# Kernel optimization log

Measured on AMD Instinct MI355X. Metric: run time of the kernel, lower is better.

Reference implementation:

```python
import jax, jax.numpy as jnp
import numpy as np

N_NODES = 100000
N_EDGES = 1600000
N_GRAPHS = 1000
F_IN, HID = 9, 64


def _glorot(key, shape):
    fan_in, fan_out = shape[0], shape[1]
    lim = (6.0 / (fan_in + fan_out)) ** 0.5
    return jax.random.uniform(key, shape, jnp.float32, -lim, lim)


def setup_inputs() -> dict:
    key = jax.random.key(0)
    ks = jax.random.split(key, 12)
    x = jax.random.normal(ks[0], (N_NODES, F_IN), jnp.float32)
    edge_index = jax.random.randint(ks[1], (2, N_EDGES), 0, N_NODES, jnp.int64)
    edge_attr = jnp.zeros((N_EDGES, 1), jnp.float32)
    batch = jnp.sort(jax.random.randint(ks[2], (N_NODES,), 0, N_GRAPHS, jnp.int64))
    # SAGEConv layer 1: 9 -> 64 (lin_l on aggregated neighbors w/ bias, lin_r on root)
    Wl1 = _glorot(ks[3], (F_IN, HID)); Wr1 = _glorot(ks[4], (F_IN, HID)); b1 = jnp.zeros((HID,), jnp.float32)
    # SAGEConv layer 2: 64 -> 64
    Wl2 = _glorot(ks[5], (HID, HID)); Wr2 = _glorot(ks[6], (HID, HID)); b2 = jnp.zeros((HID,), jnp.float32)
    # MLP readout: 64 -> 32 -> 1
    Wm1 = _glorot(ks[7], (HID, HID // 2)); bm1 = jnp.zeros((HID // 2,), jnp.float32)
    Wm2 = _glorot(ks[8], (HID // 2, 1)); bm2 = jnp.zeros((1,), jnp.float32)
    return dict(x=x, edge_index=edge_index, edge_attr=edge_attr, batch=batch,
                Wl1=Wl1, Wr1=Wr1, b1=b1, Wl2=Wl2, Wr2=Wr2, b2=b2,
                Wm1=Wm1, bm1=bm1, Wm2=Wm2, bm2=bm2)


def _sage_conv(x, src, dst, Wl, Wr, b, n_nodes):
    # mean aggregation of source-node features onto target nodes
    msgs = x[src]                                              # [E, F] gather
    s = jax.ops.segment_sum(msgs, dst, num_segments=n_nodes)   # [N, F] scatter-add
    cnt = jax.ops.segment_sum(jnp.ones((src.shape[0],), x.dtype), dst, num_segments=n_nodes)
    agg = s / jnp.maximum(cnt, 1.0)[:, None]
    return agg @ Wl + x @ Wr + b


def reference(x, edge_index, edge_attr, batch,
              Wl1, Wr1, b1, Wl2, Wr2, b2, Wm1, bm1, Wm2, bm2):
    src, dst = edge_index[0], edge_index[1]
    n = x.shape[0]
    h = jax.nn.relu(_sage_conv(x, src, dst, Wl1, Wr1, b1, n))
    h = _sage_conv(h, src, dst, Wl2, Wr2, b2, n)               # no act after last layer
    # global mean pool over graphs
    gs = jax.ops.segment_sum(h, batch, num_segments=N_GRAPHS)
    gc = jax.ops.segment_sum(jnp.ones((n,), h.dtype), batch, num_segments=N_GRAPHS)
    xg = gs / jnp.maximum(gc, 1.0)[:, None]                    # [G, 64]
    out = jax.nn.sigmoid(jax.nn.relu(xg @ Wm1 + bm1) @ Wm2 + bm2)  # [G, 1]
    return out
```

## Files before the change

### kernel.cpp

```cpp
#include <hip/hip_runtime.h>
#include <math.h>

#define N_NODES  100000
#define N_EDGES  1600000
#define N_GRAPHS 1000
#define F_IN     9
#define HID      64
#define NBUCK    196
#define BCAP     12288
#define CHUNK    4096

typedef unsigned int uint32;
typedef float v2f __attribute__((ext_vector_type(2)));


__device__ __forceinline__ uint32 pk_lo(float a, float b, uint32 old) {
    return (uint32)__builtin_amdgcn_cvt_pk_fp8_f32(a, b, (int)old, false);
}
__device__ __forceinline__ uint32 pk_hi(float a, float b, uint32 old) {
    return (uint32)__builtin_amdgcn_cvt_pk_fp8_f32(a, b, (int)old, true);
}

__global__ __launch_bounds__(256) void pad_part_kernel(const float* __restrict__ x,
                                                       const int* __restrict__ ei,
                                                       int* __restrict__ gcur,
                                                       int2* __restrict__ ebuf,
                                                       uint32* __restrict__ x8b) {
    __shared__ int lcnt[NBUCK], lbase[NBUCK];
    int tid = threadIdx.x;

    int n = blockIdx.x * 256 + tid;
    if (n < N_NODES) {
        uint32 w[4];
        #pragma unroll
        for (int p = 0; p < 4; ++p) {
            float v0 = (4 * p + 0 < F_IN) ? x[(size_t)n * F_IN + 4 * p + 0] : 0.0f;
            float v1 = (4 * p + 1 < F_IN) ? x[(size_t)n * F_IN + 4 * p + 1] : 0.0f;
            float v2 = (4 * p + 2 < F_IN) ? x[(size_t)n * F_IN + 4 * p + 2] : 0.0f;
            float v3 = (4 * p + 3 < F_IN) ? x[(size_t)n * F_IN + 4 * p + 3] : 0.0f;
            w[p] = pk_hi(v2, v3, pk_lo(v0, v1, 0u));
        }
        *reinterpret_cast<uint4*>(&x8b[(size_t)n * 4]) =
            make_uint4(w[0], w[1], w[2], w[3]);
    }

    for (int i = tid; i < NBUCK; i += 256) lcnt[i] = 0;
    __syncthreads();
    int e0 = blockIdx.x * CHUNK;
    int e1 = e0 + CHUNK; if (e1 > N_EDGES) e1 = N_EDGES;
    for (int e = e0 + tid; e < e1; e += 256)
        atomicAdd(&lcnt[ei[N_EDGES + e] >> 9], 1);
    __syncthreads();
    for (int i = tid; i < NBUCK; i += 256)
        lbase[i] = atomicAdd(&gcur[i], lcnt[i]);
    __syncthreads();
    for (int i = tid; i < NBUCK; i += 256) lcnt[i] = 0;
    __syncthreads();
    for (int e = e0 + tid; e < e1; e += 256) {
        int src = ei[e];
        int dst = ei[N_EDGES + e];
        int b = dst >> 9;
        int pos = lbase[b] + atomicAdd(&lcnt[b], 1);
        if (pos < BCAP)
            ebuf[(size_t)b * BCAP + pos] = make_int2(src, dst);
    }
}

__global__ __launch_bounds__(512) void build_csr_kernel(const int2* __restrict__ ebuf,
                                                        const int* __restrict__ gcur,
                                                        int2* __restrict__ rowcnt,
                                                        int* __restrict__ col) {
    __shared__ int cnt[512];
    __shared__ int cur[512];
    __shared__ int wsum[8];
    int b = blockIdx.x;
    int n0 = b << 9;
    int tid = threadIdx.x;
    int ec = gcur[b]; if (ec > BCAP) ec = BCAP;
    size_t base = (size_t)b * BCAP;
    cnt[tid] = 0;
    __syncthreads();
    for (int e = tid; e < ec; e += 512)
        atomicAdd(&cnt[ebuf[base + e].y - n0], 1);
    __syncthreads();
    int v = cnt[tid];
    int lane = tid & 63, wid = tid >> 6;
    int s = v;
    #pragma unroll
    for (int off = 1; off < 64; off <<= 1) {
        int u = __shfl_up(s, off, 64);
        if (lane >= off) s += u;
    }
    if (lane == 63) wsum[wid] = s;
    __syncthreads();
    int add = 0;
    for (int w = 0; w < wid; ++w) add += wsum[w];
    int off_ex = s - v + add;
    int n = n0 + tid;
    if (n < N_NODES) rowcnt[n] = make_int2((int)base + off_ex, v);
    cur[tid] = off_ex;
    __syncthreads();
    for (int e = tid; e < ec; e += 512) {
        int2 sd = ebuf[base + e];
        int pos = atomicAdd(&cur[sd.y - n0], 1);
        col[base + pos] = sd.x;
    }
}

__global__ __launch_bounds__(256) void agg_l1_kernel(const float* __restrict__ x,
                                                     const uint32* __restrict__ x8b,
                                                     const int2* __restrict__ rowcnt,
                                                     const int* __restrict__ col,
                                                     const float* __restrict__ Wl1,
                                                     const float* __restrict__ Wr1,
                                                     const float* __restrict__ b1,
                                                     const int* __restrict__ batch,
                                                     uint32* __restrict__ h1b,
                                                     float* __restrict__ poolH) {
    __shared__ float w1s[F_IN * 128];
    __shared__ float bs[HID];
    __shared__ float ss[64 * 17];
    __shared__ float xs[64 * 10];
    __shared__ float hs[64 * 65];
    int tid = threadIdx.x;
    int n0 = blockIdx.x * 64;
    for (int i = tid; i < F_IN * HID; i += 256) {
        int f = i >> 6, j = i & 63;
        w1s[f * 128 + j]      = Wl1[i];
        w1s[f * 128 + 64 + j] = Wr1[i];
    }
    if (tid < HID) bs[tid] = b1[tid];
    for (int i = tid; i < 64 * F_IN; i += 256) {
        int r = i / F_IN, f = i - r * F_IN;
        int n = n0 + r;
        xs[r * 10 + f] = (n < N_NODES) ? x[(size_t)n * F_IN + f] : 0.0f;
    }

    {
        int r = tid >> 2, q = tid & 3;
        int n = n0 + r;
        float4 a = make_float4(0.f, 0.f, 0.f, 0.f);
        if (n < N_NODES) {
            int2 rc = rowcnt[n];
            #pragma unroll 4
            for (int i = 0; i < rc.y; ++i) {
                int c = col[rc.x + i];
                uint32 d = x8b[(size_t)c * 4 + q];
                v2f f0 = __builtin_amdgcn_cvt_pk_f32_fp8((int)d, false);
                v2f f1 = __builtin_amdgcn_cvt_pk_f32_fp8((int)d, true);
                a.x += f0[0]; a.y += f0[1];
                a.z += f1[0]; a.w += f1[1];
            }
            float inv = 1.0f / fmaxf((float)rc.y, 1.0f);
            a.x *= inv; a.y *= inv; a.z *= inv; a.w *= inv;
        }
        int q4 = q * 4;
        ss[r * 17 + q4 + 0] = a.x;
        ss[r * 17 + q4 + 1] = a.y;
        ss[r * 17 + q4 + 2] = a.z;
        ss[r * 17 + q4 + 3] = a.w;
    }
    __syncthreads();

    int r = tid >> 2, cg = tid & 3, k0 = cg * 16;
    float h[16];
    #pragma unroll
    for (int kk = 0; kk < 16; ++kk) {
        int k = k0 + kk;
        float v = bs[k];
        #pragma unroll
        for (int f = 0; f < F_IN; ++f)
            v += ss[r * 17 + f] * w1s[f * 128 + k]
               + xs[r * 10 + f] * w1s[f * 128 + 64 + k];
        v = fmaxf(v, 0.0f);
        h[kk] = v;
        hs[r * 65 + k] = v;
    }
    int n = n0 + r;
    if (n < N_NODES) {
        uint32 w[4];
        #pragma unroll
        for (int p = 0; p < 4; ++p)
            w[p] = pk_hi(h[4 * p + 2], h[4 * p + 3],
                         pk_lo(h[4 * p + 0], h[4 * p + 1], 0u));
        *reinterpret_cast<uint4*>(&h1b[(size_t)n * 16 + cg * 4]) =
            make_uint4(w[0], w[1], w[2], w[3]);
    }
    __syncthreads();
    if (tid < HID) {
        int j = tid;
        int cur = batch[(n0 < N_NODES) ? n0 : (N_NODES - 1)];
        float v = (n0 < N_NODES) ? hs[0 * 65 + j] : 0.0f;
        for (int rr = 1; rr < 64; ++rr) {
            int nn = n0 + rr;
            bool ok = (nn < N_NODES);
            int g = batch[ok ? nn : (N_NODES - 1)];
            float val = ok ? hs[rr * 65 + j] : 0.0f;
            if (g == cur) v += val;
            else { atomicAdd(&poolH[cur * HID + j], v); cur = g; v = val; }
        }
        atomicAdd(&poolH[cur * HID + j], v);
    }
}

__global__ __launch_bounds__(1024) void gather2_kernel(const uint32* __restrict__ h1b,
                                                       const int2* __restrict__ rowcnt,
                                                       const int* __restrict__ col,
                                                       const int* __restrict__ batch,
                                                       float* __restrict__ poolA) {
    __shared__ float sh[16][HID];
    int w = threadIdx.x >> 6;
    int lane = threadIdx.x & 63;
    int slot = lane >> 3;
    int grp  = lane & 7;
    int n = blockIdx.x * 16 + w;
    int2 rc = rowcnt[n];
    float a[8];
    #pragma unroll
    for (int k = 0; k < 8; ++k) a[k] = 0.0f;
    #pragma unroll 2
    for (int i = slot; i < rc.y; i += 8) {
        int c = col[rc.x + i];
        uint2 d = *reinterpret_cast<const uint2*>(&h1b[(size_t)c * 16 + grp * 2]);
        v2f f0 = __builtin_amdgcn_cvt_pk_f32_fp8((int)d.x, false);
        v2f f1 = __builtin_amdgcn_cvt_pk_f32_fp8((int)d.x, true);
        v2f f2 = __builtin_amdgcn_cvt_pk_f32_fp8((int)d.y, false);
        v2f f3 = __builtin_amdgcn_cvt_pk_f32_fp8((int)d.y, true);
        a[0] += f0[0]; a[1] += f0[1];
        a[2] += f1[0]; a[3] += f1[1];
        a[4] += f2[0]; a[5] += f2[1];
        a[6] += f3[0]; a[7] += f3[1];
    }
    #pragma unroll
    for (int k = 0; k < 8; ++k) {
        a[k] += __shfl_xor(a[k], 8, 64);
        a[k] += __shfl_xor(a[k], 16, 64);
        a[k] += __shfl_xor(a[k], 32, 64);
    }
    float inv = 1.0f / fmaxf((float)rc.y, 1.0f);
    if (slot == 0) {
        #pragma unroll
        for (int k = 0; k < 8; ++k)
            sh[w][grp * 8 + k] = a[k] * inv;
    }
    __syncthreads();
    if (threadIdx.x < HID) {
        int j = threadIdx.x;
        int base = blockIdx.x * 16;
        int cur = batch[base];
        float v = sh[0][j];
        for (int r = 1; r < 16; ++r) {
            int g = batch[base + r];
            float val = sh[r][j];
            if (g == cur) v += val;
            else { atomicAdd(&poolA[cur * HID + j], v); cur = g; v = val; }
        }
        atomicAdd(&poolA[cur * HID + j], v);
    }
}

__global__ void mlp_kernel(const float* __restrict__ poolA,
                           const float* __restrict__ poolH,
                           const int* __restrict__ batch,
                           const float* __restrict__ Wl2,
                           const float* __restrict__ Wr2,
                           const float* __restrict__ b2,
                           const float* __restrict__ Wm1,
                           const float* __restrict__ bm1,
                           const float* __restrict__ Wm2,
                           const float* __restrict__ bm2,
                           float* __restrict__ out) {
    __shared__ float spA[4][HID], spH[4][HID], sx[4][HID];
    int t = blockIdx.x * blockDim.x + threadIdx.x;
    int g = t >> 6;
    int j = t & 63;
    int w = threadIdx.x >> 6;
    if (g >= N_GRAPHS) return;
    int lo = 0, hi = N_NODES;
    while (lo < hi) { int m = (lo + hi) >> 1; if (batch[m] < g) lo = m + 1; else hi = m; }
    int start = lo;
    lo = 0; hi = N_NODES;
    while (lo < hi) { int m = (lo + hi) >> 1; if (batch[m] < g + 1) lo = m + 1; else hi = m; }
    int cntg = lo - start;
    float inv = 1.0f / fmaxf((float)cntg, 1.0f);
    spA[w][j] = poolA[g * HID + j];
    spH[w][j] = poolH[g * HID + j];
    float acc = 0.0f;
    #pragma unroll 8
    for (int k = 0; k < HID; ++k)
        acc += spA[w][k] * Wl2[k * HID + j] + spH[w][k] * Wr2[k * HID + j];
    sx[w][j] = acc * inv + b2[j];
    if (j < 32) {
        float a = bm1[j];
        #pragma unroll 8
        for (int k = 0; k < HID; ++k)
            a += sx[w][k] * Wm1[k * 32 + j];
        float r = fmaxf(a, 0.0f) * Wm2[j];
        #pragma unroll
        for (int off = 16; off > 0; off >>= 1)
            r += __shfl_down(r, off, 32);
        if (j == 0)
            out[g] = 1.0f / (1.0f + expf(-(r + bm2[0])));
    }
}

extern "C" void kernel_launch(void* const* d_in, const int* in_sizes, int n_in,
                              void* d_out, int out_size, void* d_ws, size_t ws_size,
                              hipStream_t stream) {
    const float* x    = (const float*)d_in[0];
    const int*   ei   = (const int*)d_in[1];
    const int*   batch= (const int*)d_in[3];
    const float* Wl1  = (const float*)d_in[4];
    const float* Wr1  = (const float*)d_in[5];
    const float* b1   = (const float*)d_in[6];
    const float* Wl2  = (const float*)d_in[7];
    const float* Wr2  = (const float*)d_in[8];
    const float* b2   = (const float*)d_in[9];
    const float* Wm1  = (const float*)d_in[10];
    const float* bm1  = (const float*)d_in[11];
    const float* Wm2  = (const float*)d_in[12];
    const float* bm2  = (const float*)d_in[13];
    float* out = (float*)d_out;

    int*   wsi = (int*)d_ws;
    float* wsf = (float*)d_ws;
    float*  poolA  = wsf;
    float*  poolH  = wsf + 64000;
    int*    gcur   = wsi + 128000;
    int2*   rowcnt = (int2*)(wsi + 128200);
    int*    col    = wsi + 328204;
    int2*   ebuf   = (int2*)(wsi + 2736652);
    uint32* x8b    = (uint32*)(wsi + 7553548);
    uint32* h1b    = (uint32*)(wsi + 7953548);

    hipMemsetAsync(d_ws, 0, 128200 * sizeof(int), stream);

    {   int bl = (N_EDGES + CHUNK - 1) / CHUNK;
        pad_part_kernel<<<bl, 256, 0, stream>>>(x, ei, gcur, ebuf, x8b);
    }
    build_csr_kernel<<<NBUCK, 512, 0, stream>>>(ebuf, gcur, rowcnt, col);
    {   int th = 256, bl = (N_NODES + 63) / 64;
        agg_l1_kernel<<<bl, th, 0, stream>>>(x, x8b, rowcnt, col, Wl1, Wr1, b1,
                                             batch, h1b, poolH);
    }
    {   int th = 1024, bl = N_NODES / 16;
        gather2_kernel<<<bl, th, 0, stream>>>(h1b, rowcnt, col, batch, poolA);
    }
    {   int th = 256, bl = (N_GRAPHS * 64) / th;
        mlp_kernel<<<bl, th, 0, stream>>>(poolA, poolH, batch,
                                          Wl2, Wr2, b2, Wm1, bm1, Wm2, bm2, out);
    }
}
```

Measured before the change: 154.1 us.

## Split fp8 hidden features into four column chunks to shrink the gather working set

Layer-1 outputs are now stored chunk-major: four planes of 16 fp8 features (16 bytes per node per plane) instead of 64 bytes per node row. The layer-2 gather runs four times as many blocks, each handling one feature chunk with 4-byte loads and 16 edge slots per wave. The aim is a per-pass gathered array of about 1.6 MB that stays cache-resident, which improves random-access hit rates. In exchange, col and rowcnt are re-read four times, the loads are narrower, there are four times more pooling atomics, and an extra shuffle reduction step is added.

```diff
diff --git a/kernel.cpp b/kernel.cpp
--- a/kernel.cpp
+++ b/kernel.cpp
@@ -9,6 +9,7 @@
 #define NBUCK    196
 #define BCAP     12288
 #define CHUNK    4096
+#define NGRP2    6250
 
 typedef unsigned int uint32;
 typedef float v2f __attribute__((ext_vector_type(2)));
@@ -115,7 +116,7 @@
                                                      const float* __restrict__ Wr1,
                                                      const float* __restrict__ b1,
                                                      const int* __restrict__ batch,
-                                                     uint32* __restrict__ h1b,
+                                                     uint32* __restrict__ h1c,
                                                      float* __restrict__ poolH) {
     __shared__ float w1s[F_IN * 128];
     __shared__ float bs[HID];
@@ -183,7 +184,7 @@
         for (int p = 0; p < 4; ++p)
             w[p] = pk_hi(h[4 * p + 2], h[4 * p + 3],
                          pk_lo(h[4 * p + 0], h[4 * p + 1], 0u));
-        *reinterpret_cast<uint4*>(&h1b[(size_t)n * 16 + cg * 4]) =
+        *reinterpret_cast<uint4*>(&h1c[((size_t)cg * N_NODES + n) * 4]) =
             make_uint4(w[0], w[1], w[2], w[3]);
     }
     __syncthreads();
@@ -203,36 +204,36 @@
     }
 }
 
-__global__ __launch_bounds__(1024) void gather2_kernel(const uint32* __restrict__ h1b,
+__global__ __launch_bounds__(1024) void gather2_kernel(const uint32* __restrict__ h1c,
                                                        const int2* __restrict__ rowcnt,
                                                        const int* __restrict__ col,
                                                        const int* __restrict__ batch,
                                                        float* __restrict__ poolA) {
-    __shared__ float sh[16][HID];
+    __shared__ float sh[16][16];
+    int chunk = blockIdx.x / NGRP2;
+    int ngrp  = blockIdx.x - chunk * NGRP2;
     int w = threadIdx.x >> 6;
     int lane = threadIdx.x & 63;
-    int slot = lane >> 3;
-    int grp  = lane & 7;
-    int n = blockIdx.x * 16 + w;
+    int slot = lane >> 2;
+    int dw   = lane & 3;
+    int n = ngrp * 16 + w;
     int2 rc = rowcnt[n];
-    float a[8];
+    const uint32* hbase = h1c + (size_t)chunk * N_NODES * 4 + dw;
+    float a[4];
     #pragma unroll
-    for (int k = 0; k < 8; ++k) a[k] = 0.0f;
+    for (int k = 0; k < 4; ++k) a[k] = 0.0f;
     #pragma unroll 2
-    for (int i = slot; i < rc.y; i += 8) {
+    for (int i = slot; i < rc.y; i += 16) {
         int c = col[rc.x + i];
-        uint2 d = *reinterpret_cast<const uint2*>(&h1b[(size_t)c * 16 + grp * 2]);
-        v2f f0 = __builtin_amdgcn_cvt_pk_f32_fp8((int)d.x, false);
-        v2f f1 = __builtin_amdgcn_cvt_pk_f32_fp8((int)d.x, true);
-        v2f f2 = __builtin_amdgcn_cvt_pk_f32_fp8((int)d.y, false);
-        v2f f3 = __builtin_amdgcn_cvt_pk_f32_fp8((int)d.y, true);
+        uint32 d = hbase[(size_t)c * 4];
+        v2f f0 = __builtin_amdgcn_cvt_pk_f32_fp8((int)d, false);
+        v2f f1 = __builtin_amdgcn_cvt_pk_f32_fp8((int)d, true);
         a[0] += f0[0]; a[1] += f0[1];
         a[2] += f1[0]; a[3] += f1[1];
-        a[4] += f2[0]; a[5] += f2[1];
-        a[6] += f3[0]; a[7] += f3[1];
     }
     #pragma unroll
-    for (int k = 0; k < 8; ++k) {
+    for (int k = 0; k < 4; ++k) {
+        a[k] += __shfl_xor(a[k], 4, 64);
         a[k] += __shfl_xor(a[k], 8, 64);
         a[k] += __shfl_xor(a[k], 16, 64);
         a[k] += __shfl_xor(a[k], 32, 64);
@@ -240,22 +241,23 @@
     float inv = 1.0f / fmaxf((float)rc.y, 1.0f);
     if (slot == 0) {
         #pragma unroll
-        for (int k = 0; k < 8; ++k)
-            sh[w][grp * 8 + k] = a[k] * inv;
-    }
-    __syncthreads();
-    if (threadIdx.x < HID) {
+        for (int k = 0; k < 4; ++k)
+            sh[w][dw * 4 + k] = a[k] * inv;
+    }
+    __syncthreads();
+    if (threadIdx.x < 16) {
         int j = threadIdx.x;
-        int base = blockIdx.x * 16;
+        int base = ngrp * 16;
+        int jj = chunk * 16 + j;
         int cur = batch[base];
         float v = sh[0][j];
         for (int r = 1; r < 16; ++r) {
             int g = batch[base + r];
             float val = sh[r][j];
             if (g == cur) v += val;
-            else { atomicAdd(&poolA[cur * HID + j], v); cur = g; v = val; }
+            else { atomicAdd(&poolA[cur * HID + jj], v); cur = g; v = val; }
         }
-        atomicAdd(&poolA[cur * HID + j], v);
+        atomicAdd(&poolA[cur * HID + jj], v);
     }
 }
 
@@ -331,7 +333,7 @@
     int*    col    = wsi + 328204;
     int2*   ebuf   = (int2*)(wsi + 2736652);
     uint32* x8b    = (uint32*)(wsi + 7553548);
-    uint32* h1b    = (uint32*)(wsi + 7953548);
+    uint32* h1c    = (uint32*)(wsi + 7953548);
 
     hipMemsetAsync(d_ws, 0, 128200 * sizeof(int), stream);
 
@@ -341,10 +343,10 @@
     build_csr_kernel<<<NBUCK, 512, 0, stream>>>(ebuf, gcur, rowcnt, col);
     {   int th = 256, bl = (N_NODES + 63) / 64;
         agg_l1_kernel<<<bl, th, 0, stream>>>(x, x8b, rowcnt, col, Wl1, Wr1, b1,
-                                             batch, h1b, poolH);
-    }
-    {   int th = 1024, bl = N_NODES / 16;
-        gather2_kernel<<<bl, th, 0, stream>>>(h1b, rowcnt, col, batch, poolA);
+                                             batch, h1c, poolH);
+    }
+    {   int th = 1024, bl = 4 * NGRP2;
+        gather2_kernel<<<bl, th, 0, stream>>>(h1c, rowcnt, col, batch, poolA);
     }
     {   int th = 256, bl = (N_GRAPHS * 64) / th;
         mlp_kernel<<<bl, th, 0, stream>>>(poolA, poolH, batch,
```

Result: slower. 253.4 us (+64.4%).

## Pack edge buffer, fuse layer-1 aggregation into CSR build, retile gather2

Applied to the files above, without the earlier changes.

Each edge in the bucket buffer is now packed into one int (17-bit src plus 9-bit local dst) instead of an int2, which halves that traffic. The layer-1 neighbor aggregation moves into build_csr_kernel as LDS float atomics per bucket, writing normalized means to a new s16 buffer. The new l1_kernel only does the dense transform. gather2 now uses 256-thread blocks of 4 nodes with a two-way unrolled loop and packed v2f accumulators. The risks are heavy LDS atomic contention on only 196 blocks, lower parallelism for the aggregation, and the extra s16 round trip.

```diff
diff --git a/kernel.cpp b/kernel.cpp
--- a/kernel.cpp
+++ b/kernel.cpp
@@ -24,7 +24,7 @@
 __global__ __launch_bounds__(256) void pad_part_kernel(const float* __restrict__ x,
                                                        const int* __restrict__ ei,
                                                        int* __restrict__ gcur,
-                                                       int2* __restrict__ ebuf,
+                                                       int* __restrict__ ebuf,
                                                        uint32* __restrict__ x8b) {
     __shared__ int lcnt[NBUCK], lbase[NBUCK];
     int tid = threadIdx.x;
@@ -62,26 +62,30 @@
         int b = dst >> 9;
         int pos = lbase[b] + atomicAdd(&lcnt[b], 1);
         if (pos < BCAP)
-            ebuf[(size_t)b * BCAP + pos] = make_int2(src, dst);
-    }
-}
-
-__global__ __launch_bounds__(512) void build_csr_kernel(const int2* __restrict__ ebuf,
+            ebuf[(size_t)b * BCAP + pos] = src | ((dst & 511) << 17);
+    }
+}
+
+__global__ __launch_bounds__(512) void build_csr_kernel(const int* __restrict__ ebuf,
                                                         const int* __restrict__ gcur,
+                                                        const uint32* __restrict__ x8b,
                                                         int2* __restrict__ rowcnt,
-                                                        int* __restrict__ col) {
+                                                        int* __restrict__ col,
+                                                        float* __restrict__ s16) {
     __shared__ int cnt[512];
     __shared__ int cur[512];
     __shared__ int wsum[8];
+    __shared__ float xacc[512 * 16];
     int b = blockIdx.x;
     int n0 = b << 9;
     int tid = threadIdx.x;
     int ec = gcur[b]; if (ec > BCAP) ec = BCAP;
     size_t base = (size_t)b * BCAP;
     cnt[tid] = 0;
+    for (int i = tid; i < 512 * 16; i += 512) xacc[i] = 0.0f;
     __syncthreads();
     for (int e = tid; e < ec; e += 512)
-        atomicAdd(&cnt[ebuf[base + e].y - n0], 1);
+        atomicAdd(&cnt[(uint32)ebuf[base + e] >> 17], 1);
     __syncthreads();
     int v = cnt[tid];
     int lane = tid & 63, wid = tid >> 6;
@@ -101,22 +105,45 @@
     cur[tid] = off_ex;
     __syncthreads();
     for (int e = tid; e < ec; e += 512) {
-        int2 sd = ebuf[base + e];
-        int pos = atomicAdd(&cur[sd.y - n0], 1);
-        col[base + pos] = sd.x;
-    }
-}
-
-__global__ __launch_bounds__(256) void agg_l1_kernel(const float* __restrict__ x,
-                                                     const uint32* __restrict__ x8b,
-                                                     const int2* __restrict__ rowcnt,
-                                                     const int* __restrict__ col,
-                                                     const float* __restrict__ Wl1,
-                                                     const float* __restrict__ Wr1,
-                                                     const float* __restrict__ b1,
-                                                     const int* __restrict__ batch,
-                                                     uint32* __restrict__ h1b,
-                                                     float* __restrict__ poolH) {
+        int pv = ebuf[base + e];
+        int src = pv & 0x1FFFF;
+        int ld  = (uint32)pv >> 17;
+        int pos = atomicAdd(&cur[ld], 1);
+        col[base + pos] = src;
+    }
+    for (int idx = tid; idx < ec * 4; idx += 512) {
+        int e = idx >> 2, q = idx & 3;
+        int pv = ebuf[base + e];
+        int src = pv & 0x1FFFF;
+        int ld  = (uint32)pv >> 17;
+        uint32 d = x8b[(size_t)src * 4 + q];
+        v2f f0 = __builtin_amdgcn_cvt_pk_f32_fp8((int)d, false);
+        v2f f1 = __builtin_amdgcn_cvt_pk_f32_fp8((int)d, true);
+        float* xa = &xacc[ld * 16 + q * 4];
+        atomicAdd(&xa[0], f0[0]);
+        atomicAdd(&xa[1], f0[1]);
+        atomicAdd(&xa[2], f1[0]);
+        atomicAdd(&xa[3], f1[1]);
+    }
+    __syncthreads();
+    for (int i = tid; i < 512 * 16; i += 512) {
+        int r = i >> 4;
+        int nn = n0 + r;
+        if (nn < N_NODES) {
+            float inv = 1.0f / fmaxf((float)cnt[r], 1.0f);
+            s16[(size_t)nn * 16 + (i & 15)] = xacc[i] * inv;
+        }
+    }
+}
+
+__global__ __launch_bounds__(256) void l1_kernel(const float* __restrict__ x,
+                                                 const float* __restrict__ s16,
+                                                 const float* __restrict__ Wl1,
+                                                 const float* __restrict__ Wr1,
+                                                 const float* __restrict__ b1,
+                                                 const int* __restrict__ batch,
+                                                 uint32* __restrict__ h1b,
+                                                 float* __restrict__ poolH) {
     __shared__ float w1s[F_IN * 128];
     __shared__ float bs[HID];
     __shared__ float ss[64 * 17];
@@ -130,35 +157,15 @@
         w1s[f * 128 + 64 + j] = Wr1[i];
     }
     if (tid < HID) bs[tid] = b1[tid];
+    for (int i = tid; i < 64 * 16; i += 256) {
+        int r = i >> 4, f = i & 15;
+        int n = n0 + r;
+        ss[r * 17 + f] = (n < N_NODES) ? s16[(size_t)n * 16 + f] : 0.0f;
+    }
     for (int i = tid; i < 64 * F_IN; i += 256) {
         int r = i / F_IN, f = i - r * F_IN;
         int n = n0 + r;
         xs[r * 10 + f] = (n < N_NODES) ? x[(size_t)n * F_IN + f] : 0.0f;
-    }
-
-    {
-        int r = tid >> 2, q = tid & 3;
-        int n = n0 + r;
-        float4 a = make_float4(0.f, 0.f, 0.f, 0.f);
-        if (n < N_NODES) {
-            int2 rc = rowcnt[n];
-            #pragma unroll 4
-            for (int i = 0; i < rc.y; ++i) {
-                int c = col[rc.x + i];
-                uint32 d = x8b[(size_t)c * 4 + q];
-                v2f f0 = __builtin_amdgcn_cvt_pk_f32_fp8((int)d, false);
-                v2f f1 = __builtin_amdgcn_cvt_pk_f32_fp8((int)d, true);
-                a.x += f0[0]; a.y += f0[1];
-                a.z += f1[0]; a.w += f1[1];
-            }
-            float inv = 1.0f / fmaxf((float)rc.y, 1.0f);
-            a.x *= inv; a.y *= inv; a.z *= inv; a.w *= inv;
-        }
-        int q4 = q * 4;
-        ss[r * 17 + q4 + 0] = a.x;
-        ss[r * 17 + q4 + 1] = a.y;
-        ss[r * 17 + q4 + 2] = a.z;
-        ss[r * 17 + q4 + 3] = a.w;
     }
     __syncthreads();
 
@@ -203,53 +210,65 @@
     }
 }
 
-__global__ __launch_bounds__(1024) void gather2_kernel(const uint32* __restrict__ h1b,
-                                                       const int2* __restrict__ rowcnt,
-                                                       const int* __restrict__ col,
-                                                       const int* __restrict__ batch,
-                                                       float* __restrict__ poolA) {
-    __shared__ float sh[16][HID];
+__global__ __launch_bounds__(256) void gather2_kernel(const uint32* __restrict__ h1b,
+                                                      const int2* __restrict__ rowcnt,
+                                                      const int* __restrict__ col,
+                                                      const int* __restrict__ batch,
+                                                      float* __restrict__ poolA) {
+    __shared__ float sh[4][HID];
     int w = threadIdx.x >> 6;
     int lane = threadIdx.x & 63;
     int slot = lane >> 3;
     int grp  = lane & 7;
-    int n = blockIdx.x * 16 + w;
+    int n = blockIdx.x * 4 + w;
     int2 rc = rowcnt[n];
-    float a[8];
-    #pragma unroll
-    for (int k = 0; k < 8; ++k) a[k] = 0.0f;
-    #pragma unroll 2
-    for (int i = slot; i < rc.y; i += 8) {
-        int c = col[rc.x + i];
-        uint2 d = *reinterpret_cast<const uint2*>(&h1b[(size_t)c * 16 + grp * 2]);
-        v2f f0 = __builtin_amdgcn_cvt_pk_f32_fp8((int)d.x, false);
-        v2f f1 = __builtin_amdgcn_cvt_pk_f32_fp8((int)d.x, true);
-        v2f f2 = __builtin_amdgcn_cvt_pk_f32_fp8((int)d.y, false);
-        v2f f3 = __builtin_amdgcn_cvt_pk_f32_fp8((int)d.y, true);
-        a[0] += f0[0]; a[1] += f0[1];
-        a[2] += f1[0]; a[3] += f1[1];
-        a[4] += f2[0]; a[5] += f2[1];
-        a[6] += f3[0]; a[7] += f3[1];
-    }
+    const uint32* hb = h1b + grp * 2;
+    v2f a0 = {0.f, 0.f}, a1 = {0.f, 0.f}, a2 = {0.f, 0.f}, a3 = {0.f, 0.f};
+    int i = rc.x + slot;
+    int end = rc.x + rc.y;
+    for (; i + 8 < end; i += 16) {
+        int c0 = col[i];
+        int c1 = col[i + 8];
+        uint2 d0 = *reinterpret_cast<const uint2*>(hb + (size_t)c0 * 16);
+        uint2 d1 = *reinterpret_cast<const uint2*>(hb + (size_t)c1 * 16);
+        a0 += __builtin_amdgcn_cvt_pk_f32_fp8((int)d0.x, false);
+        a1 += __builtin_amdgcn_cvt_pk_f32_fp8((int)d0.x, true);
+        a2 += __builtin_amdgcn_cvt_pk_f32_fp8((int)d0.y, false);
+        a3 += __builtin_amdgcn_cvt_pk_f32_fp8((int)d0.y, true);
+        a0 += __builtin_amdgcn_cvt_pk_f32_fp8((int)d1.x, false);
+        a1 += __builtin_amdgcn_cvt_pk_f32_fp8((int)d1.x, true);
+        a2 += __builtin_amdgcn_cvt_pk_f32_fp8((int)d1.y, false);
+        a3 += __builtin_amdgcn_cvt_pk_f32_fp8((int)d1.y, true);
+    }
+    if (i < end) {
+        int c0 = col[i];
+        uint2 d0 = *reinterpret_cast<const uint2*>(hb + (size_t)c0 * 16);
+        a0 += __builtin_amdgcn_cvt_pk_f32_fp8((int)d0.x, false);
+        a1 += __builtin_amdgcn_cvt_pk_f32_fp8((int)d0.x, true);
+        a2 += __builtin_amdgcn_cvt_pk_f32_fp8((int)d0.y, false);
+        a3 += __builtin_amdgcn_cvt_pk_f32_fp8((int)d0.y, true);
+    }
+    float r8[8] = {a0[0], a0[1], a1[0], a1[1], a2[0], a2[1], a3[0], a3[1]};
     #pragma unroll
     for (int k = 0; k < 8; ++k) {
-        a[k] += __shfl_xor(a[k], 8, 64);
-        a[k] += __shfl_xor(a[k], 16, 64);
-        a[k] += __shfl_xor(a[k], 32, 64);
+        r8[k] += __shfl_xor(r8[k], 8, 64);
+        r8[k] += __shfl_xor(r8[k], 16, 64);
+        r8[k] += __shfl_xor(r8[k], 32, 64);
     }
     float inv = 1.0f / fmaxf((float)rc.y, 1.0f);
     if (slot == 0) {
         #pragma unroll
         for (int k = 0; k < 8; ++k)
-            sh[w][grp * 8 + k] = a[k] * inv;
+            sh[w][grp * 8 + k] = r8[k] * inv;
     }
     __syncthreads();
     if (threadIdx.x < HID) {
         int j = threadIdx.x;
-        int base = blockIdx.x * 16;
+        int base = blockIdx.x * 4;
         int cur = batch[base];
         float v = sh[0][j];
-        for (int r = 1; r < 16; ++r) {
+        #pragma unroll
+        for (int r = 1; r < 4; ++r) {
             int g = batch[base + r];
             float val = sh[r][j];
             if (g == cur) v += val;
@@ -328,22 +347,22 @@
     float*  poolH  = wsf + 64000;
     int*    gcur   = wsi + 128000;
     int2*   rowcnt = (int2*)(wsi + 128200);
-    int*    col    = wsi + 328204;
-    int2*   ebuf   = (int2*)(wsi + 2736652);
-    uint32* x8b    = (uint32*)(wsi + 7553548);
-    uint32* h1b    = (uint32*)(wsi + 7953548);
+    int*    col    = wsi + 328200;
+    int*    ebuf   = wsi + 2736648;
+    uint32* x8b    = (uint32*)(wsi + 5145096);
+    float*  s16    = wsf + 5545096;
+    uint32* h1b    = (uint32*)(wsi + 7145096);
 
     hipMemsetAsync(d_ws, 0, 128200 * sizeof(int), stream);
 
     {   int bl = (N_EDGES + CHUNK - 1) / CHUNK;
         pad_part_kernel<<<bl, 256, 0, stream>>>(x, ei, gcur, ebuf, x8b);
     }
-    build_csr_kernel<<<NBUCK, 512, 0, stream>>>(ebuf, gcur, rowcnt, col);
+    build_csr_kernel<<<NBUCK, 512, 0, stream>>>(ebuf, gcur, x8b, rowcnt, col, s16);
     {   int th = 256, bl = (N_NODES + 63) / 64;
-        agg_l1_kernel<<<bl, th, 0, stream>>>(x, x8b, rowcnt, col, Wl1, Wr1, b1,
-                                             batch, h1b, poolH);
-    }
-    {   int th = 1024, bl = N_NODES / 16;
+        l1_kernel<<<bl, th, 0, stream>>>(x, s16, Wl1, Wr1, b1, batch, h1b, poolH);
+    }
+    {   int th = 256, bl = N_NODES / 4;
         gather2_kernel<<<bl, th, 0, stream>>>(h1b, rowcnt, col, batch, poolA);
     }
     {   int th = 256, bl = (N_GRAPHS * 64) / th;
```

Measured after the change: 301.5 us. 1.96x slower.
